# Kernel tuning notes

Hardware: AMD Instinct MI355X
Metric: run time of the kernel (lower is better)

Reference implementation:

```python
import jax, jax.numpy as jnp
import numpy as np

B, LX, LY, D, H = 16, 2048, 2048, 1024, 1024
NEG = -1e30


def setup_inputs() -> dict:
    key = jax.random.key(0)
    k1, k2, k3, k4, k5, k6 = jax.random.split(key, 6)
    x = jax.random.normal(k1, (B, LX, D), dtype=jnp.float32)
    y = jax.random.normal(k2, (B, LY, D), dtype=jnp.float32)
    x_mask = jax.random.randint(k3, (B, LX), 0, 2).astype(bool)
    y_mask = jax.random.randint(k4, (B, LY), 0, 2).astype(bool)
    # nn.Linear(D, H, bias=False) weights, shape [H, D], applied as x @ W.T
    scale = 1.0 / np.sqrt(D)
    Wx = jax.random.uniform(k5, (H, D), dtype=jnp.float32, minval=-scale, maxval=scale)
    Wy = jax.random.uniform(k6, (H, D), dtype=jnp.float32, minval=-scale, maxval=scale)
    return {"x": x, "y": y, "x_mask": x_mask, "y_mask": y_mask, "Wx": Wx, "Wy": Wy}


def reference(x, y, x_mask, y_mask, Wx, Wy):
    # projections + relu
    px = jax.nn.relu(jnp.einsum('bxd,hd->bxh', x, Wx))  # [B, LX, H]
    py = jax.nn.relu(jnp.einsum('byd,hd->byh', y, Wy))  # [B, LY, H]
    # bilinear scores [B, LX, LY]
    s = jnp.einsum('bxh,byh->bxy', px, py)
    # dual masking (1 = padding)
    mask = x_mask[:, :, None] | y_mask[:, None, :]
    s = jnp.where(mask, NEG, s)
    # two softmax directions
    y_h = jnp.einsum('bxy,byd->bxd', jax.nn.softmax(s, axis=2), y)  # [B, LX, D]
    x_h = jnp.einsum('bxy,bxd->byd', jax.nn.softmax(s, axis=1), x)  # [B, LY, D]
    return (y_h, x_h)
```

## Files before the change

### kernel.cpp

```cpp
#include <hip/hip_runtime.h>
#include <stdint.h>


typedef short    short8  __attribute__((ext_vector_type(8)));
typedef _Float16 half8   __attribute__((ext_vector_type(8)));
typedef _Float16 half4   __attribute__((ext_vector_type(4)));
typedef float    floatx4 __attribute__((ext_vector_type(4)));

static __device__ __forceinline__ float b2f(unsigned short s) {
    union { unsigned int u; float f; } v; v.u = ((unsigned int)s) << 16; return v.f;
}
static __device__ __forceinline__ _Float16 f2h(float f) { return (_Float16)f; }
static __device__ __forceinline__ unsigned fenc(float f) {
    unsigned u = __float_as_uint(f);
    return (u & 0x80000000u) ? ~u : (u | 0x80000000u);
}
static __device__ __forceinline__ float fdec(unsigned u) {
    return __uint_as_float((u & 0x80000000u) ? (u ^ 0x80000000u) : ~u);
}
#define ENC_NEGINF 0x007FFFFFu

static __device__ __forceinline__ void gl_lds16(const _Float16* g, _Float16* l) {
    __builtin_amdgcn_global_load_lds(
        (const __attribute__((address_space(1))) void*)g,
        (__attribute__((address_space(3))) void*)l, 16, 0, 0);
}

__global__ void detect_kernel(const unsigned int* __restrict__ xm,
                              const unsigned int* __restrict__ xv,
                              int* __restrict__ flags)
{
    __shared__ int anyBig, cnt;
    if (threadIdx.x == 0) { anyBig = 0; cnt = 0; }
    __syncthreads();
    int big = 0;
    for (int i = threadIdx.x; i < 2048; i += 256)
        if (xm[i] > 1u) big = 1;
    if (big) atomicOr(&anyBig, 1);
    int c = 0;
    for (int i = threadIdx.x; i < 4096; i += 256) {
        const unsigned lo = xv[i] & 0xFFFFu;
        const unsigned e  = (lo >> 7) & 0xFFu;
        if ((lo & 0x7FFFu) == 0u || (e >= 96u && e <= 143u)) c++;
    }
    atomicAdd(&cnt, c);
    __syncthreads();
    if (threadIdx.x == 0) { flags[0] = anyBig; flags[1] = (cnt < 3600) ? 1 : 0; }
}

__global__ void init_kernel(unsigned* __restrict__ mr, float* __restrict__ lr,
                            unsigned* __restrict__ mc, float* __restrict__ lc, int n)
{
    const int i = blockIdx.x * 256 + threadIdx.x;
    if (i < n) { mr[i] = ENC_NEGINF; mc[i] = ENC_NEGINF; lr[i] = 0.f; lc[i] = 0.f; }
}

__global__ __launch_bounds__(256)
void transpose_in_kernel(const void* __restrict__ in, _Float16* __restrict__ out,
                         _Float16* __restrict__ outH, const int* __restrict__ flags)
{
    const int b = blockIdx.z, lt = blockIdx.y, dt = blockIdx.x;
    const int inf32 = flags[1];
    __shared__ _Float16 T[64 * 67];
    const int t  = threadIdx.x;
    const int r0 = t >> 3;
    const int c0 = (t & 7) * 8;
    const unsigned short* in16 = (const unsigned short*)in + (long long)b * 2048 * 1024;
    const float*          inf  = (const float*)in + (long long)b * 2048 * 1024;
    #pragma unroll
    for (int it = 0; it < 2; it++) {
        const int ll = r0 + it * 32;
        const long long src = (long long)(lt * 64 + ll) * 1024 + dt * 64 + c0;
        _Float16 v[8];
        if (inf32) {
            const float* p = inf + src;
            #pragma unroll
            for (int k = 0; k < 8; k++) v[k] = f2h(p[k]);
        } else {
            short8 r = *(const short8*)(in16 + src);
            #pragma unroll
            for (int k = 0; k < 8; k++) v[k] = f2h(b2f((unsigned short)r[k]));
        }
        if (outH) {
            half8 o;
            #pragma unroll
            for (int k = 0; k < 8; k++) o[k] = v[k];
            *(half8*)&outH[(long long)b * 2048 * 1024 + src] = o;
        }
        #pragma unroll
        for (int k = 0; k < 8; k++) T[(c0 + k) * 67 + ll] = v[k];
    }
    __syncthreads();
    #pragma unroll
    for (int it = 0; it < 2; it++) {
        const int dl = r0 + it * 32;
        half8 o;
        #pragma unroll
        for (int k = 0; k < 8; k++) o[k] = T[dl * 67 + c0 + k];
        *(half8*)&out[(long long)b * 1024 * 2048 +
                      (long long)(dt * 64 + dl) * 2048 + lt * 64 + c0] = o;
    }
}

__global__ __launch_bounds__(256)
void cvt16_kernel(const void* __restrict__ in, _Float16* __restrict__ out,
                  const int* __restrict__ flags, long long n)
{
    const long long i = (((long long)blockIdx.x * 256) + threadIdx.x) << 3;
    if (i >= n) return;
    half8 o;
    if (flags[1]) {
        const float* pf = (const float*)in + i;
        #pragma unroll
        for (int k = 0; k < 8; k++) o[k] = f2h(pf[k]);
    } else {
        short8 rr = *(const short8*)((const unsigned short*)in + i);
        #pragma unroll
        for (int k = 0; k < 8; k++) o[k] = f2h(b2f((unsigned short)rr[k]));
    }
    *(half8*)&out[i] = o;
}

__global__ __launch_bounds__(256)
void transform_kernel(const float* __restrict__ s,
                      _Float16* __restrict__ Pr, _Float16* __restrict__ Pct,
                      const unsigned* __restrict__ mrow_u,
                      const unsigned* __restrict__ mcol_u,
                      float* __restrict__ lrow, float* __restrict__ lcol, int gb0)
{
    const int b  = blockIdx.z;
    const int xt = blockIdx.y;
    const int yt = blockIdx.x;
    const long long sb  = (long long)b * 2048 * 2048;
    const int gbL = (gb0 + b) * 2048;
    __shared__ _Float16 T[64 * 67];
    const int t   = threadIdx.x;
    const int rl  = t >> 4;
    const int cl  = (t & 15) * 4;
    const int gy0 = yt * 64 + cl;
    float mc[4];
    #pragma unroll
    for (int j = 0; j < 4; j++) mc[j] = fdec(mcol_u[gbL + gy0 + j]);
    #pragma unroll
    for (int step = 0; step < 4; step++) {
        const int xl = rl + step * 16;
        const int gx = xt * 64 + xl;
        const float mr = fdec(mrow_u[gbL + gx]);
        const floatx4 v = *(const floatx4*)&s[sb + (long long)gx * 2048 + gy0];
        float er[4];
        #pragma unroll
        for (int j = 0; j < 4; j++) er[j] = __expf(v[j] - mr);
        half4 h;
        #pragma unroll
        for (int j = 0; j < 4; j++) h[j] = f2h(er[j]);
        *(half4*)&Pr[sb + (long long)gx * 2048 + gy0] = h;
        float rs = er[0] + er[1] + er[2] + er[3];
        rs += __shfl_xor(rs, 1); rs += __shfl_xor(rs, 2);
        rs += __shfl_xor(rs, 4); rs += __shfl_xor(rs, 8);
        if ((t & 15) == 0) atomicAdd(&lrow[gbL + gx], rs);
        #pragma unroll
        for (int j = 0; j < 4; j++)
            T[(cl + j) * 67 + xl] = f2h(__expf(v[j] - mc[j]));
    }
    __syncthreads();
    #pragma unroll
    for (int it = 0; it < 2; it++) {
        const int yl = (t >> 3) + it * 32;
        const int x0 = (t & 7) * 8;
        half8 o; float cs = 0.f;
        #pragma unroll
        for (int k = 0; k < 8; k++) { _Float16 e = T[yl * 67 + x0 + k]; o[k] = e; cs += (float)e; }
        *(half8*)&Pct[sb + (long long)(yt * 64 + yl) * 2048 + xt * 64 + x0] = o;
        cs += __shfl_xor(cs, 1); cs += __shfl_xor(cs, 2); cs += __shfl_xor(cs, 4);
        if ((t & 7) == 0) atomicAdd(&lcol[gbL + yt * 64 + yl], cs);
    }
}

#define BAR   __builtin_amdgcn_s_barrier()
#define WAITL0 asm volatile("s_waitcnt lgkmcnt(0)" ::: "memory")
#define WAITV4 asm volatile("s_waitcnt vmcnt(4)" ::: "memory")
#define WAITV0 asm volatile("s_waitcnt vmcnt(0)" ::: "memory")

#define PHASE_READ_A(KHOFF, G)                                                 \
    _Pragma("unroll") for (int i = 0; i < 4; i++)                              \
        af[i] = *(const half8*)&S[ab + (KHOFF) + aBase + (G) * 2048 + i * 512];
#define PHASE_READ_B(KHOFF)                                                    \
    _Pragma("unroll") for (int j = 0; j < 4; j++)                              \
        bfr[j] = *(const half8*)&S[ab + (KHOFF) + bBase + j * 512];
#define MFMA_G(G)                                                              \
    _Pragma("unroll") for (int i = 0; i < 4; i++)                              \
        _Pragma("unroll") for (int j = 0; j < 4; j++)                          \
            acc[(G) * 4 + i][j] = __builtin_amdgcn_mfma_f32_16x16x32_f16(      \
                af[i], bfr[j], acc[(G) * 4 + i][j], 0, 0, 0);
#define STAGE_A(KOFF, BH)                                                      \
    { gl_lds16(a0 + (KOFF), &S[(BH) + eh]);                                    \
      gl_lds16(a1 + (KOFF), &S[(BH) + 4096 + eh]); }
#define STAGE_B(KOFF, BH)                                                      \
    { gl_lds16(bp0 + (KOFF), &S[32768 + (BH) + eh]);                           \
      gl_lds16(bp1 + (KOFF), &S[32768 + (BH) + 4096 + eh]); }

template<int EPI>
__global__ __launch_bounds__(512, 2)
void gemm256_kernel(const _Float16* __restrict__ Agv, const _Float16* __restrict__ Bgv,
                    void* __restrict__ Cgv,
                    unsigned* __restrict__ mrow_u, unsigned* __restrict__ mcol_u,
                    const float* __restrict__ lsum,
                    const int* __restrict__ xmask, const int* __restrict__ ymask,
                    const int* __restrict__ gflags, int gb0,
                    int K, int lda, int ldb, int ldc,
                    long long saA, long long saB, long long saC, int statL)
{
    __shared__ _Float16 S[65536];

    const int gx = gridDim.x, gy = gridDim.y;
    const int nwg = gx * gy * (int)gridDim.z;
    int flat = ((int)blockIdx.z * gy + (int)blockIdx.y) * gx + (int)blockIdx.x;
    {
        const int q = nwg >> 3, r = nwg & 7, xc = flat & 7, o = flat >> 3;
        flat = (xc < r ? xc * (q + 1) : r * (q + 1) + (xc - r) * q) + o;
    }
    const int bx = flat % gx;
    const int by = (flat / gx) % gy;
    const int b  = flat / (gx * gy);

    const _Float16* Ag = Agv + (long long)b * saA;
    const _Float16* Bg = Bgv + (long long)b * saB;
    const int m0 = by << 8, n0 = bx << 8;

    const int t    = threadIdx.x;
    const int lane = t & 63;
    const int wave = t >> 6;
    const int wr   = wave >> 2;
    const int wc   = wave & 3;
    const int l16  = lane & 15;
    const int quad = lane >> 4;

    const int e0 = t << 4;
    const int eh = e0 >> 1;
    const int r0 = e0 >> 6;
    const int ch = (((e0 & 63) ^ ((r0 & 3) << 4)) >> 1);
    const _Float16* a0  = Ag + (long long)(m0 + r0) * lda + ch;
    const _Float16* a1  = Ag + (long long)(m0 + r0 + 128) * lda + ch;
    const _Float16* bp0 = Bg + (long long)(n0 + r0) * ldb + ch;
    const _Float16* bp1 = Bg + (long long)(n0 + r0 + 128) * ldb + ch;

    const int colh  = (quad << 3) ^ ((l16 & 3) << 3);
    const int aBase = (wr * 128 + l16) * 32 + colh;
    const int bBase = 32768 + (wc * 64 + l16) * 32 + colh;

    floatx4 acc[8][4];
    #pragma unroll
    for (int i = 0; i < 8; i++)
        #pragma unroll
        for (int j = 0; j < 4; j++)
            acc[i][j] = (floatx4){0.f, 0.f, 0.f, 0.f};

    const int NT = K >> 6;

    STAGE_A(0, 0); STAGE_B(0, 0); STAGE_A(32, 8192); STAGE_B(32, 8192);
    WAITV4;
    BAR;

    int buf = 0;
    for (int tt = 0; tt < NT; ++tt) {
        const bool more = (tt + 1 < NT);
        const int nk = (tt + 1) << 6;
        const int ab = buf << 14;
        const int nb = (buf ^ 1) << 14;
        half8 af[4], bfr[4];

        PHASE_READ_A(0, 0); PHASE_READ_B(0);
        if (more) STAGE_A(nk, nb);
        BAR; WAITL0;
        __builtin_amdgcn_s_setprio(1); MFMA_G(0); __builtin_amdgcn_s_setprio(0);
        BAR;
        PHASE_READ_A(0, 1);
        if (more) STAGE_B(nk, nb);
        BAR; WAITL0;
        __builtin_amdgcn_s_setprio(1); MFMA_G(1); __builtin_amdgcn_s_setprio(0);
        if (more) { WAITV4; } else { WAITV0; }
        BAR;
        PHASE_READ_A(8192, 0); PHASE_READ_B(8192);
        if (more) STAGE_A(nk + 32, nb + 8192);
        BAR; WAITL0;
        __builtin_amdgcn_s_setprio(1); MFMA_G(0); __builtin_amdgcn_s_setprio(0);
        BAR;
        PHASE_READ_A(8192, 1);
        if (more) STAGE_B(nk + 32, nb + 8192);
        BAR; WAITL0;
        __builtin_amdgcn_s_setprio(1); MFMA_G(1); __builtin_amdgcn_s_setprio(0);
        if (more) { WAITV4; }
        BAR;
        buf ^= 1;
    }

    const int rowbase = m0 + wr * 128 + quad * 4;
    const int colbase = n0 + wc * 64 + l16;

    if (EPI == 0) {
        _Float16* C = (_Float16*)Cgv + (long long)b * saC;
        #pragma unroll
        for (int i = 0; i < 8; i++)
            #pragma unroll
            for (int j = 0; j < 4; j++)
                #pragma unroll
                for (int r = 0; r < 4; r++)
                    C[(long long)(rowbase + i * 16 + r) * ldc + colbase + j * 16] =
                        f2h(fmaxf(acc[i][j][r], 0.f));
    } else if (EPI == 3) {
        float* C = (float*)Cgv + (long long)b * saC;
        const float* ls = lsum + (long long)(gb0 + b) * statL;
        #pragma unroll
        for (int i = 0; i < 8; i++) {
            #pragma unroll
            for (int r = 0; r < 4; r++) {
                const int grow = rowbase + i * 16 + r;
                const float inv = 1.0f / ls[grow];
                #pragma unroll
                for (int j = 0; j < 4; j++)
                    C[(long long)grow * ldc + colbase + j * 16] = acc[i][j][r] * inv;
            }
        }
    } else {
        float* C = (float*)Cgv + (long long)b * saC;
        const int u8 = gflags[0];
        const unsigned char* xm8 = (const unsigned char*)xmask;
        const unsigned char* ym8 = (const unsigned char*)ymask;
        const long long sx = (long long)(gb0 + b) * statL;
        bool cmk[4];
        #pragma unroll
        for (int j = 0; j < 4; j++) {
            const int gcol = colbase + j * 16;
            cmk[j] = u8 ? (xm8 != nullptr && ym8[sx + gcol] != 0)
                        : (ymask[sx + gcol] != 0);
        }
        float colmax[4] = {-1e38f, -1e38f, -1e38f, -1e38f};
        #pragma unroll
        for (int i = 0; i < 8; i++) {
            #pragma unroll
            for (int r = 0; r < 4; r++) {
                const int grow = rowbase + i * 16 + r;
                const bool rm = u8 ? (xm8[sx + grow] != 0) : (xmask[sx + grow] != 0);
                float rowmax = -1e38f;
                #pragma unroll
                for (int j = 0; j < 4; j++) {
                    float v = acc[i][j][r];
                    v = (rm || cmk[j]) ? -1e30f : v;
                    C[(long long)grow * ldc + colbase + j * 16] = v;
                    rowmax = fmaxf(rowmax, v);
                    colmax[j] = fmaxf(colmax[j], v);
                }
                rowmax = fmaxf(rowmax, __shfl_xor(rowmax, 1));
                rowmax = fmaxf(rowmax, __shfl_xor(rowmax, 2));
                rowmax = fmaxf(rowmax, __shfl_xor(rowmax, 4));
                rowmax = fmaxf(rowmax, __shfl_xor(rowmax, 8));
                if (l16 == 0) atomicMax(&mrow_u[sx + grow], fenc(rowmax));
            }
        }
        #pragma unroll
        for (int j = 0; j < 4; j++) {
            float cm = colmax[j];
            cm = fmaxf(cm, __shfl_xor(cm, 16));
            cm = fmaxf(cm, __shfl_xor(cm, 32));
            if (quad == 0) atomicMax(&mcol_u[sx + colbase + j * 16], fenc(cm));
        }
    }
}

__global__ __launch_bounds__(256, 2)
void gemm_proj_raw(const void* __restrict__ Agv, const void* __restrict__ Bgv,
                   _Float16* __restrict__ Cg, const int* __restrict__ gflags,
                   int K, int lda, int ldb, int ldc)
{
    const int inf32 = gflags[1];
    const unsigned short* Ag16 = (const unsigned short*)Agv;
    const float*          Agf  = (const float*)Agv;
    const unsigned short* Bg16 = (const unsigned short*)Bgv;
    const float*          Bgf  = (const float*)Bgv;

    __shared__ _Float16 As[128 * 64];
    __shared__ _Float16 Bs[128 * 64];

    const int t = threadIdx.x, lane = t & 63, wave = t >> 6;
    const int wm = (wave >> 1) << 6, wn = (wave & 1) << 6;
    const int l16 = lane & 15, quad = lane >> 4;
    const int m0 = blockIdx.y * 128, n0 = blockIdx.x * 128;

    floatx4 acc[4][4];
    #pragma unroll
    for (int i = 0; i < 4; i++)
        #pragma unroll
        for (int j = 0; j < 4; j++)
            acc[i][j] = (floatx4){0.f, 0.f, 0.f, 0.f};

    for (int k0 = 0; k0 < K; k0 += 64) {
        #pragma unroll
        for (int c = t; c < 128 * 8; c += 256) {
            const int row = c >> 3, kc = (c & 7) << 3;
            half8 o;
            if (inf32) {
                const float* src = Agf + (long long)(m0 + row) * lda + k0 + kc;
                #pragma unroll
                for (int j = 0; j < 8; j++) o[j] = f2h(src[j]);
            } else {
                short8 r = *(const short8*)(Ag16 + (long long)(m0 + row) * lda + k0 + kc);
                #pragma unroll
                for (int j = 0; j < 8; j++) o[j] = f2h(b2f((unsigned short)r[j]));
            }
            *(half8*)&As[row * 64 + kc] = o;
        }
        #pragma unroll
        for (int c = t; c < 128 * 8; c += 256) {
            const int row = c >> 3, kc = (c & 7) << 3;
            half8 o;
            if (inf32) {
                const float* src = Bgf + (long long)(n0 + row) * ldb + k0 + kc;
                #pragma unroll
                for (int j = 0; j < 8; j++) o[j] = f2h(src[j]);
            } else {
                short8 r = *(const short8*)(Bg16 + (long long)(n0 + row) * ldb + k0 + kc);
                #pragma unroll
                for (int j = 0; j < 8; j++) o[j] = f2h(b2f((unsigned short)r[j]));
            }
            *(half8*)&Bs[row * 64 + kc] = o;
        }
        __syncthreads();
        #pragma unroll
        for (int kk = 0; kk < 64; kk += 32) {
            half8 af[4], bfr[4];
            #pragma unroll
            for (int i = 0; i < 4; i++)
                af[i] = *(const half8*)&As[(wm + i * 16 + l16) * 64 + kk + quad * 8];
            #pragma unroll
            for (int i = 0; i < 4; i++)
                bfr[i] = *(const half8*)&Bs[(wn + i * 16 + l16) * 64 + kk + quad * 8];
            #pragma unroll
            for (int i = 0; i < 4; i++)
                #pragma unroll
                for (int j = 0; j < 4; j++)
                    acc[i][j] = __builtin_amdgcn_mfma_f32_16x16x32_f16(af[i], bfr[j], acc[i][j], 0, 0, 0);
        }
        __syncthreads();
    }
    #pragma unroll
    for (int i = 0; i < 4; i++)
        #pragma unroll
        for (int j = 0; j < 4; j++)
            #pragma unroll
            for (int r = 0; r < 4; r++)
                Cg[(long long)(m0 + wm + i * 16 + quad * 4 + r) * ldc + n0 + wn + j * 16 + l16] =
                    f2h(fmaxf(acc[i][j][r], 0.f));
}

extern "C" void kernel_launch(void* const* d_in, const int* in_sizes, int n_in,
                              void* d_out, int out_size, void* d_ws, size_t ws_size,
                              hipStream_t stream)
{
    const int B = 16, L = 2048, D = 1024, H = 1024;
    const void* x  = d_in[0];
    const void* y  = d_in[1];
    const int* xmask = (const int*)d_in[2];
    const int* ymask = (const int*)d_in[3];
    const void* Wx = d_in[4];
    const void* Wy = d_in[5];

    _Float16* px = (_Float16*)d_ws;
    _Float16* py = px + (size_t)B * L * H;
    _Float16* xT = py + (size_t)B * L * H;
    _Float16* yT = xT + (size_t)B * D * L;
    unsigned* mrow_u = (unsigned*)(yT + (size_t)B * D * L);
    float*    lrow   = (float*)(mrow_u + (size_t)B * L);
    unsigned* mcol_u = (unsigned*)(lrow + (size_t)B * L);
    float*    lcol   = (float*)(mcol_u + (size_t)B * L);
    int*      flags  = (int*)(lcol + (size_t)B * L);
    char*     p0     = (char*)(flags + 16);

    const long long per_batch = (long long)L * L * 4 + 2LL * L * L * 2;
    const long long wlen = (long long)H * D;
    const long long xlen = (long long)B * L * D;
    const long long fixed = (long long)(p0 - (char*)d_ws);
    const long long fast_extra = 2 * wlen * 2 + 2 * xlen * 2;

    const bool fast = ((long long)ws_size - fixed - fast_extra) >= per_batch;
    _Float16 *WxH = nullptr, *WyH = nullptr, *xH = nullptr, *yH = nullptr;
    char* dynbase = p0;
    if (fast) {
        WxH = (_Float16*)p0;
        WyH = WxH + wlen;
        xH  = WyH + wlen;
        yH  = xH + xlen;
        dynbase = (char*)(yH + xlen);
    }
    long long avail = (long long)ws_size - (long long)(dynbase - (char*)d_ws);
    int nc = (int)(avail / per_batch);
    if (nc < 1) nc = 1;
    if (nc > B) nc = B;

    float*    s   = (float*)dynbase;
    _Float16* Pr  = (_Float16*)(s + (size_t)nc * L * L);
    _Float16* Pct = Pr + (size_t)nc * L * L;

    float* yh = (float*)d_out;
    float* xh = yh + (size_t)B * L * D;

    dim3 blk(256);

    detect_kernel<<<1, 256, 0, stream>>>((const unsigned int*)xmask,
                                         (const unsigned int*)x, flags);
    init_kernel<<<dim3((B * L + 255) / 256), blk, 0, stream>>>(mrow_u, lrow, mcol_u, lcol, B * L);
    transpose_in_kernel<<<dim3(D / 64, L / 64, B), blk, 0, stream>>>(x, xT, xH, flags);
    transpose_in_kernel<<<dim3(D / 64, L / 64, B), blk, 0, stream>>>(y, yT, yH, flags);

    if (fast) {
        cvt16_kernel<<<dim3((int)(wlen / 2048)), blk, 0, stream>>>(Wx, WxH, flags, wlen);
        cvt16_kernel<<<dim3((int)(wlen / 2048)), blk, 0, stream>>>(Wy, WyH, flags, wlen);
        gemm256_kernel<0><<<dim3(H / 256, (B * L) / 256, 1), dim3(512), 0, stream>>>(
            xH, WxH, px, nullptr, nullptr, nullptr, nullptr, nullptr, flags, 0,
            D, D, D, H, 0, 0, 0, 0);
        gemm256_kernel<0><<<dim3(H / 256, (B * L) / 256, 1), dim3(512), 0, stream>>>(
            yH, WyH, py, nullptr, nullptr, nullptr, nullptr, nullptr, flags, 0,
            D, D, D, H, 0, 0, 0, 0);
    } else {
        gemm_proj_raw<<<dim3(H / 128, (B * L) / 128, 1), blk, 0, stream>>>(
            x, Wx, px, flags, D, D, D, H);
        gemm_proj_raw<<<dim3(H / 128, (B * L) / 128, 1), blk, 0, stream>>>(
            y, Wy, py, flags, D, D, D, H);
    }

    for (int b0 = 0; b0 < B; b0 += nc) {
        const int cur = (B - b0 < nc) ? (B - b0) : nc;
        gemm256_kernel<1><<<dim3(L / 256, L / 256, cur), dim3(512), 0, stream>>>(
            px + (size_t)b0 * L * H, py + (size_t)b0 * L * H, s,
            mrow_u, mcol_u, nullptr, xmask, ymask, flags, b0,
            H, H, H, L, (long long)L * H, (long long)L * H, (long long)L * L, L);
        transform_kernel<<<dim3(L / 64, L / 64, cur), blk, 0, stream>>>(
            s, Pr, Pct, mrow_u, mcol_u, lrow, lcol, b0);
        gemm256_kernel<3><<<dim3(D / 256, L / 256, cur), dim3(512), 0, stream>>>(
            Pr, yT + (size_t)b0 * D * L, yh + (size_t)b0 * L * D,
            nullptr, nullptr, lrow, nullptr, nullptr, flags, b0,
            L, L, L, D, (long long)L * L, (long long)D * L, (long long)L * D, L);
        gemm256_kernel<3><<<dim3(D / 256, L / 256, cur), dim3(512), 0, stream>>>(
            Pct, xT + (size_t)b0 * D * L, xh + (size_t)b0 * L * D,
            nullptr, nullptr, lcol, nullptr, nullptr, flags, b0,
            L, L, L, D, (long long)L * L, (long long)D * L, (long long)L * D, L);
    }
    (void)in_sizes; (void)n_in; (void)out_size; (void)ws_size;
}
```

Measured before the change: 1.291 ms.

## Peel last K-tile, issue LDS stages before reads, and change LDS swizzle

The main GEMM loop now runs NT-1 iterations without the per-step 'more' checks, and the final tile is peeled into its own block. Global-to-LDS stage loads are now issued before the LDS fragment reads, and the explicit lgkmcnt(0) waits are removed, leaving the compiler to order LDS waits. The XOR swizzle now keys on (row>>1)&3 instead of row&3, which is meant to reduce LDS bank conflicts for 16-byte fragment reads. Relying on compiler-inserted waits and on removed barriers in the peeled tail risks ordering problems if the schedule changes.

```diff
diff --git a/kernel.cpp b/kernel.cpp
--- a/kernel.cpp
+++ b/kernel.cpp
@@ -177,7 +177,6 @@
 }
 
 #define BAR   __builtin_amdgcn_s_barrier()
-#define WAITL0 asm volatile("s_waitcnt lgkmcnt(0)" ::: "memory")
 #define WAITV4 asm volatile("s_waitcnt vmcnt(4)" ::: "memory")
 #define WAITV0 asm volatile("s_waitcnt vmcnt(0)" ::: "memory")
 
@@ -238,13 +237,13 @@
     const int e0 = t << 4;
     const int eh = e0 >> 1;
     const int r0 = e0 >> 6;
-    const int ch = (((e0 & 63) ^ ((r0 & 3) << 4)) >> 1);
+    const int ch = (((e0 & 63) ^ (((r0 >> 1) & 3) << 4)) >> 1);
     const _Float16* a0  = Ag + (long long)(m0 + r0) * lda + ch;
     const _Float16* a1  = Ag + (long long)(m0 + r0 + 128) * lda + ch;
     const _Float16* bp0 = Bg + (long long)(n0 + r0) * ldb + ch;
     const _Float16* bp1 = Bg + (long long)(n0 + r0 + 128) * ldb + ch;
 
-    const int colh  = (quad << 3) ^ ((l16 & 3) << 3);
+    const int colh  = (quad << 3) ^ (((l16 >> 1) & 3) << 3);
     const int aBase = (wr * 128 + l16) * 32 + colh;
     const int bBase = 32768 + (wc * 64 + l16) * 32 + colh;
 
@@ -262,36 +261,52 @@
     BAR;
 
     int buf = 0;
-    for (int tt = 0; tt < NT; ++tt) {
-        const bool more = (tt + 1 < NT);
+    for (int tt = 0; tt < NT - 1; ++tt) {
         const int nk = (tt + 1) << 6;
         const int ab = buf << 14;
         const int nb = (buf ^ 1) << 14;
         half8 af[4], bfr[4];
 
+        STAGE_A(nk, nb);
         PHASE_READ_A(0, 0); PHASE_READ_B(0);
-        if (more) STAGE_A(nk, nb);
-        BAR; WAITL0;
+        BAR;
         __builtin_amdgcn_s_setprio(1); MFMA_G(0); __builtin_amdgcn_s_setprio(0);
         BAR;
+        STAGE_B(nk, nb);
         PHASE_READ_A(0, 1);
-        if (more) STAGE_B(nk, nb);
-        BAR; WAITL0;
+        BAR;
         __builtin_amdgcn_s_setprio(1); MFMA_G(1); __builtin_amdgcn_s_setprio(0);
-        if (more) { WAITV4; } else { WAITV0; }
-        BAR;
+        WAITV4;
+        BAR;
+        STAGE_A(nk + 32, nb + 8192);
         PHASE_READ_A(8192, 0); PHASE_READ_B(8192);
-        if (more) STAGE_A(nk + 32, nb + 8192);
-        BAR; WAITL0;
+        BAR;
         __builtin_amdgcn_s_setprio(1); MFMA_G(0); __builtin_amdgcn_s_setprio(0);
         BAR;
+        STAGE_B(nk + 32, nb + 8192);
         PHASE_READ_A(8192, 1);
-        if (more) STAGE_B(nk + 32, nb + 8192);
-        BAR; WAITL0;
+        BAR;
         __builtin_amdgcn_s_setprio(1); MFMA_G(1); __builtin_amdgcn_s_setprio(0);
-        if (more) { WAITV4; }
+        WAITV4;
         BAR;
         buf ^= 1;
+    }
+
+    {
+        const int ab = buf << 14;
+        half8 af[4], bfr[4];
+        PHASE_READ_A(0, 0); PHASE_READ_B(0);
+        BAR;
+        __builtin_amdgcn_s_setprio(1); MFMA_G(0); __builtin_amdgcn_s_setprio(0);
+        BAR;
+        PHASE_READ_A(0, 1);
+        __builtin_amdgcn_s_setprio(1); MFMA_G(1); __builtin_amdgcn_s_setprio(0);
+        WAITV0;
+        BAR;
+        PHASE_READ_A(8192, 0); PHASE_READ_B(8192);
+        __builtin_amdgcn_s_setprio(1); MFMA_G(0); __builtin_amdgcn_s_setprio(0);
+        PHASE_READ_A(8192, 1);
+        __builtin_amdgcn_s_setprio(1); MFMA_G(1); __builtin_amdgcn_s_setprio(0);
     }
 
     const int rowbase = m0 + wr * 128 + quad * 4;
@@ -331,7 +346,7 @@
         #pragma unroll
         for (int j = 0; j < 4; j++) {
             const int gcol = colbase + j * 16;
-            cmk[j] = u8 ? (xm8 != nullptr && ym8[sx + gcol] != 0)
+            cmk[j] = u8 ? (ym8[sx + gcol] != 0)
                         : (ymask[sx + gcol] != 0);
         }
         float colmax[4] = {-1e38f, -1e38f, -1e38f, -1e38f};
```

Result: faster. 1.254 ms (-2.9%).
